# Optimization experiments

Measured on AMD Instinct MI355X. Metric: run time of the kernel, lower is better.

The kernel has to match this reference:

```python
import math
import jax, jax.numpy as jnp
import numpy as np

N = 2048          # batch size
D = 256           # embedding_dim
MEM = 16384       # memory_size
ANOMALY_WEIGHT = 1.0
TEMP = 0.1
MOMENTUM = 0.01
NCLS = 2          # binary phishing labels -> max(labels.max()+1, 2) == 2


def setup_inputs() -> dict:
    key = jax.random.key(0)
    ks = jax.random.split(key, 10)
    s = 1.0 / math.sqrt(D)  # nn.Linear default init range
    return {
        'z': jax.random.normal(ks[0], (N, D), jnp.float32),
        'labels': jax.random.randint(ks[1], (N,), 0, NCLS),
        'memory': jax.random.normal(ks[2], (MEM, D), jnp.float32),
        'memory_weights': jax.random.uniform(ks[3], (MEM,), jnp.float32),
        'running_mean': jnp.zeros((D,), jnp.float32),
        'running_cov': jnp.eye(D, dtype=jnp.float32),
        'Wq': jax.random.uniform(ks[4], (D, D), jnp.float32, -s, s),
        'bq': jax.random.uniform(ks[5], (D,), jnp.float32, -s, s),
        'Wk': jax.random.uniform(ks[6], (D, D), jnp.float32, -s, s),
        'bk': jax.random.uniform(ks[7], (D,), jnp.float32, -s, s),
        'Wv': jax.random.uniform(ks[8], (D, D), jnp.float32, -s, s),
        'bv': jax.random.uniform(ks[9], (D,), jnp.float32, -s, s),
    }


def reference(z, labels, memory, memory_weights, running_mean, running_cov,
              Wq, bq, Wk, bk, Wv, bv):
    # ---- update(z.detach(), labels): entire update path is detached in torch ----
    z_sg = jax.lax.stop_gradient(z)

    # _update_stats: EMA of batch mean / covariance (done before importance)
    mu = z_sg.mean(axis=0)                                  # [D]
    zc = z_sg - mu
    cov = zc.T @ zc / max(N - 1, 1)                         # [D, D]
    rm = (1.0 - MOMENTUM) * running_mean + MOMENTUM * mu
    rc = (1.0 - MOMENTUM) * running_cov + MOMENTUM * cov

    # _mahalanobis with updated running stats
    c = z_sg - rm
    cov_inv = jnp.linalg.inv(rc + 1e-6 * jnp.eye(D, dtype=rc.dtype))
    dist = jnp.sqrt(jnp.clip(jnp.einsum('nd,de,ne->n', c, cov_inv, c), 1e-8))
    a_norm = (dist - dist.min()) / (dist.max() - dist.min() + 1e-8)

    # _mi_proxy: KL(batch label dist || uniform), broadcast to all items
    counts = jnp.zeros((NCLS,), z.dtype).at[labels].add(1.0)
    p = counts / jnp.clip(counts.sum(), 1.0)
    # p / uniform == p * NCLS; clip inside log for safety (both classes present)
    kl = jnp.clip((p * jnp.log(jnp.clip(p * NCLS, 1e-8))).sum(), 0.0)
    importance = (1.0 + ANOMALY_WEIGHT * a_norm) * kl       # [N]

    # serial top-1 priority-queue eviction, in descending-importance order
    order = jnp.argsort(-importance)
    z_ord = z_sg[order]
    imp_ord = importance[order]

    def evict_step(state, inp):
        mem, w = state
        zi, imp = inp
        j = jnp.argmin(w)                   # weakest memory slot
        rep = imp > w[j]
        mem = mem.at[j].set(jnp.where(rep, zi, mem[j]))
        w = w.at[j].set(jnp.where(rep, imp, w[j]))
        return (mem, w), None

    (mem, _), _ = jax.lax.scan(evict_step, (memory, memory_weights), (z_ord, imp_ord))

    # ---- query(z): cross-attention over the (full) updated memory ----
    Q = z @ Wq.T + bq                       # [N, D]
    K = mem @ Wk.T + bk                     # [MEM, D]
    V = mem @ Wv.T + bv                     # [MEM, D]
    sc = (Q @ K.T) / math.sqrt(D)           # [N, MEM]
    attn = jax.nn.softmax(sc / TEMP, axis=-1)
    return z + 0.5 * (attn @ V)
```

## Files before the change

kernel.cpp:

```cpp
#include <hip/hip_runtime.h>
#include <math.h>

#define NB   2048
#define DE   256
#define MEMN 16384
#define CAND_CAP 256
#define FSPL 32
#define FKPS 512
#define FIT  16

typedef __attribute__((ext_vector_type(8)))  short  short8;
typedef __attribute__((ext_vector_type(16))) float  float16;
typedef __attribute__((ext_vector_type(4)))  unsigned uint4v;
typedef __attribute__((ext_vector_type(2)))  unsigned uint2v;

static const size_t OFF_QB   = 0;
static const size_t OFF_KB   = 262144;
static const size_t OFF_VTB  = 2359296;
static const size_t OFF_LP   = 4456448;
static const size_t OFF_OPB  = 4521984;
static const size_t SO_A    = 0;
static const size_t SO_X    = 65536;
static const size_t SO_MUP  = 131072;
static const size_t SO_DIST = 147456;

__device__ inline unsigned short f2bf(float f) {
  unsigned u = __float_as_uint(f);
  unsigned r = (u + 0x7fffu + ((u >> 16) & 1u)) >> 16;
  return (unsigned short)r;
}
__device__ inline float bf2f(unsigned short s) {
  return __uint_as_float((unsigned)s << 16);
}

__device__ inline unsigned cvtpk_bf16(float lo, float hi) {
  unsigned r;
  asm("v_cvt_pk_bf16_f32 %0, %1, %2" : "=v"(r) : "v"(lo), "v"(hi));
  return r;
}

__device__ inline void halfswap(unsigned& lo, unsigned& hi, int h) {
#if __has_builtin(__builtin_amdgcn_permlane32_swap)
  (void)h;
  uint2v r = __builtin_amdgcn_permlane32_swap(lo, hi, false, false);
  lo = r.x; hi = r.y;
#else
  unsigned a = (unsigned)__shfl_xor((int)lo, 32, 64);
  unsigned b = (unsigned)__shfl_xor((int)hi, 32, 64);
  unsigned nlo = (h == 0) ? lo : b;
  unsigned nhi = (h == 0) ? a  : hi;
  lo = nlo; hi = nhi;
#endif
}

__device__ inline void bitonic_sort_u64(unsigned long long* key, int n, int tid, int nth) {
  for (int k = 2; k <= n; k <<= 1) {
    for (int j = k >> 1; j > 0; j >>= 1) {
      __syncthreads();
      for (int i = tid; i < n; i += nth) {
        int ixj = i ^ j;
        if (ixj > i) {
          unsigned long long a = key[i], b = key[ixj];
          bool up = ((i & k) == 0);
          if ((a > b) == up) { key[i] = b; key[ixj] = a; }
        }
      }
    }
  }
  __syncthreads();
}

__global__ __launch_bounds__(256) void mupart_kernel(const float* __restrict__ z,
                                                     float* __restrict__ mup,
                                                     float* __restrict__ Az) {
  int d = threadIdx.x;
  int r0 = blockIdx.x * 32;
  float4 zero4 = {0.f, 0.f, 0.f, 0.f};
  *(float4*)&Az[(size_t)blockIdx.x * 1024 + threadIdx.x * 4] = zero4;
  float s = 0.f;
  for (int r = 0; r < 32; ++r) s += z[(size_t)(r0 + r) * DE + d];
  mup[blockIdx.x * DE + d] = s;
}

__global__ __launch_bounds__(256) void covpart_kernel(const float* __restrict__ z,
                                                      float* __restrict__ A) {
  __shared__ float As[16][68];
  __shared__ float Bs[16][68];
  int tid = threadIdx.x, tx = tid & 15, ty = tid >> 4;
  int i0 = blockIdx.x * 64, j0 = blockIdx.y * 64;
  int nbase = blockIdx.z * 128;
  float acc[4][4] = {};
  for (int nt = 0; nt < 8; ++nt) {
    int n0 = nbase + nt * 16;
    for (int e = tid; e < 1024; e += 256) {
      int c = e & 63, nn = e >> 6;
      As[nn][c] = z[(size_t)(n0 + nn) * DE + i0 + c];
      Bs[nn][c] = z[(size_t)(n0 + nn) * DE + j0 + c];
    }
    __syncthreads();
#pragma unroll
    for (int nn = 0; nn < 16; ++nn) {
      float4 a4 = *(const float4*)&As[nn][ty * 4];
      float4 b4 = *(const float4*)&Bs[nn][tx * 4];
      acc[0][0] += a4.x*b4.x; acc[0][1] += a4.x*b4.y; acc[0][2] += a4.x*b4.z; acc[0][3] += a4.x*b4.w;
      acc[1][0] += a4.y*b4.x; acc[1][1] += a4.y*b4.y; acc[1][2] += a4.y*b4.z; acc[1][3] += a4.y*b4.w;
      acc[2][0] += a4.z*b4.x; acc[2][1] += a4.z*b4.y; acc[2][2] += a4.z*b4.z; acc[2][3] += a4.z*b4.w;
      acc[3][0] += a4.w*b4.x; acc[3][1] += a4.w*b4.y; acc[3][2] += a4.w*b4.z; acc[3][3] += a4.w*b4.w;
    }
    __syncthreads();
  }
  for (int r = 0; r < 4; ++r) {
    int i = i0 + ty * 4 + r;
    for (int c = 0; c < 4; ++c) {
      int j = j0 + tx * 4 + c;
      atomicAdd(&A[(size_t)i * DE + j], acc[r][c]);
    }
  }
}

__global__ __launch_bounds__(256) void gemmx_kernel(const float* __restrict__ ZtZ,
                                                    const float* __restrict__ rcov,
                                                    const float* __restrict__ mup,
                                                    float* __restrict__ X) {
  __shared__ float Ea[16][17];
  __shared__ float Eb[16][17];
  __shared__ float mus[256];
  int t = threadIdx.x, tx = t & 15, ty = t >> 4;
  int i0 = blockIdx.x * 16, j0 = blockIdx.y * 16;
  {
    float s = 0.f;
    for (int b = 0; b < 64; ++b) s += mup[b * DE + t];
    mus[t] = s;
  }
  __syncthreads();
  const float c1 = 0.01f / (float)(NB - 1);
  const float invN = 1.0f / (float)NB;
  float acc = 0.f;
  for (int k0 = 0; k0 < 256; k0 += 16) {
    int c = k0 + tx;
    {
      int r = i0 + ty;
      float base = 0.99f * rcov[(size_t)r * DE + c] +
                   c1 * (ZtZ[(size_t)r * DE + c] - mus[r] * mus[c] * invN);
      float e = -base;
      if (r == c) e += 1.0f - 1e-6f;
      Ea[ty][tx] = e;
    }
    {
      int r = j0 + ty;
      float base = 0.99f * rcov[(size_t)r * DE + c] +
                   c1 * (ZtZ[(size_t)r * DE + c] - mus[r] * mus[c] * invN);
      float e = -base;
      if (r == c) e += 1.0f - 1e-6f;
      Eb[ty][tx] = e;
    }
    __syncthreads();
#pragma unroll
    for (int k = 0; k < 16; ++k) acc += Ea[ty][k] * Eb[tx][k];
    __syncthreads();
  }
  int r = i0 + ty, c = j0 + tx;
  float base = 0.99f * rcov[(size_t)r * DE + c] +
               c1 * (ZtZ[(size_t)r * DE + c] - mus[r] * mus[c] * invN);
  float e = -base;
  if (r == c) e += 1.0f - 1e-6f;
  X[(size_t)r * DE + c] = acc + e + ((r == c) ? 1.0f : 0.0f);
}

__global__ __launch_bounds__(256) void dist_kernel(const float* __restrict__ z,
                                                   const float* __restrict__ rmean,
                                                   const float* __restrict__ mup,
                                                   const float* __restrict__ X,
                                                   float* __restrict__ dist) {
  __shared__ float cc[4][256];
  __shared__ float4 red[256];
  int n0 = blockIdx.x * 4, i = threadIdx.x;
  float s = 0.f;
  for (int b = 0; b < 64; ++b) s += mup[b * DE + i];
  float rmi = 0.99f * rmean[i] + 0.01f * s * (1.0f / (float)NB);
#pragma unroll
  for (int r = 0; r < 4; ++r) cc[r][i] = z[(size_t)(n0 + r) * DE + i] - rmi;
  __syncthreads();
  float y0 = 0.f, y1 = 0.f, y2 = 0.f, y3 = 0.f;
#pragma unroll 8
  for (int j = 0; j < DE; ++j) {
    float x = X[(size_t)j * DE + i];
    y0 += x * cc[0][j]; y1 += x * cc[1][j]; y2 += x * cc[2][j]; y3 += x * cc[3][j];
  }
  float4 v;
  v.x = y0 * cc[0][i]; v.y = y1 * cc[1][i]; v.z = y2 * cc[2][i]; v.w = y3 * cc[3][i];
  red[i] = v;
  __syncthreads();
  for (int sH = 128; sH > 0; sH >>= 1) {
    if (i < sH) {
      float4 a = red[i], b = red[i + sH];
      a.x += b.x; a.y += b.y; a.z += b.z; a.w += b.w;
      red[i] = a;
    }
    __syncthreads();
  }
  if (i < 4) {
    float4 tt = red[0];
    float d = (i == 0) ? tt.x : (i == 1) ? tt.y : (i == 2) ? tt.z : tt.w;
    dist[n0 + i] = sqrtf(fmaxf(d, 1e-8f));
  }
}

__global__ __launch_bounds__(1024) void update_kernel(const float* __restrict__ dist,
                                                      const int* __restrict__ labels,
                                                      const float* __restrict__ weights,
                                                      const float* __restrict__ z,
                                                      float* __restrict__ memory) {
  __shared__ unsigned long long ikeys[NB];
  __shared__ unsigned long long ck[CAND_CAP];
  __shared__ unsigned long long gmin[16];
  __shared__ int slots[CAND_CAP], srcs[CAND_CAP];
  __shared__ float smin[16], smax[16];
  __shared__ int scnt[16];
  __shared__ float s_kl, s_dmin, s_inv;
  __shared__ int s_ccnt, s_m, s_stop, s_bg;
  int t = threadIdx.x;
  int wid = t >> 6, lane = t & 63;

  float mn = 1e30f, mx = -1e30f; int c1 = 0;
  for (int n = t; n < NB; n += 1024) {
    float d = dist[n];
    mn = fminf(mn, d); mx = fmaxf(mx, d);
    c1 += labels[n];
  }
#pragma unroll
  for (int o = 32; o > 0; o >>= 1) {
    mn = fminf(mn, __shfl_xor(mn, o, 64));
    mx = fmaxf(mx, __shfl_xor(mx, o, 64));
    c1 += __shfl_xor(c1, o, 64);
  }
  if (lane == 0) { smin[wid] = mn; smax[wid] = mx; scnt[wid] = c1; }
  if (t == 0) { s_ccnt = 0; s_m = 0; s_stop = 0; }
  __syncthreads();
  if (t == 0) {
    float a = 1e30f, b = -1e30f; int cc = 0;
    for (int i = 0; i < 16; ++i) { a = fminf(a, smin[i]); b = fmaxf(b, smax[i]); cc += scnt[i]; }
    float p1 = (float)cc / (float)NB;
    float p0 = (float)(NB - cc) / (float)NB;
    float kl = p0 * logf(fmaxf(2.f * p0, 1e-8f)) + p1 * logf(fmaxf(2.f * p1, 1e-8f));
    s_kl = fmaxf(kl, 0.f);
    s_dmin = a;
    s_inv = 1.0f / (b - a + 1e-8f);
  }
  __syncthreads();
  float kl = s_kl;

  for (int n = t; n < NB; n += 1024) {
    float imp = (1.0f + (dist[n] - s_dmin) * s_inv) * kl;
    ikeys[n] = ((unsigned long long)(unsigned)(~__float_as_uint(imp)) << 32) | (unsigned)n;
  }
  float thresh = 2.f * kl;
  for (int j = t; j < MEMN; j += 1024) {
    float wv = weights[j];
    if (wv < thresh) {
      int p = atomicAdd(&s_ccnt, 1);
      if (p < CAND_CAP) ck[p] = ((unsigned long long)__float_as_uint(wv) << 32) | (unsigned)j;
    }
  }
  __syncthreads();
  int C = s_ccnt; if (C > CAND_CAP) C = CAND_CAP;
  for (int i = t; i < CAND_CAP; i += 1024)
    if (i >= C) ck[i] = 0xFFFFFFFFFFFFFFFFULL;
  bitonic_sort_u64(ck, CAND_CAP, t, 1024);

  {
    unsigned long long a = ikeys[wid * 128 + lane];
    unsigned long long b = ikeys[wid * 128 + 64 + lane];
    unsigned long long mm = a < b ? a : b;
#pragma unroll
    for (int o = 32; o > 0; o >>= 1) {
      unsigned long long ot = (unsigned long long)__shfl_xor((long long)mm, o, 64);
      if (ot < mm) mm = ot;
    }
    if (lane == 0) gmin[wid] = mm;
  }
  __syncthreads();

  float prevv = 0.f;
  for (int i = 0; i < C; ++i) {
    if (t == 0) {
      unsigned long long best = 0xFFFFFFFFFFFFFFFFULL;
      for (int g = 0; g < 16; ++g) if (gmin[g] < best) best = gmin[g];
      float im = __uint_as_float(~(unsigned)(best >> 32));
      float wv = __uint_as_float((unsigned)(ck[i] >> 32));
      bool ok = (im > wv) && (i == 0 || prevv >= wv);
      if (ok) {
        int idx = (int)(best & 0xffffffffULL);
        slots[s_m] = (int)(ck[i] & 0xffffffffULL);
        srcs[s_m]  = idx;
        s_m++;
        prevv = im;
        ikeys[idx] = 0xFFFFFFFFFFFFFFFFULL;
        s_bg = idx >> 7;
      } else {
        s_stop = 1; s_bg = -1;
      }
    }
    __syncthreads();
    if (s_stop) break;
    if (wid == s_bg) {
      unsigned long long a = ikeys[wid * 128 + lane];
      unsigned long long b = ikeys[wid * 128 + 64 + lane];
      unsigned long long mm = a < b ? a : b;
#pragma unroll
      for (int o = 32; o > 0; o >>= 1) {
        unsigned long long ot = (unsigned long long)__shfl_xor((long long)mm, o, 64);
        if (ot < mm) mm = ot;
      }
      if (lane == 0) gmin[wid] = mm;
    }
    __syncthreads();
  }
  int m = s_m;
  for (int e = t; e < m * DE; e += 1024) {
    int i = e >> 8, d = e & 255;
    memory[(size_t)slots[i] * DE + d] = z[(size_t)srcs[i] * DE + d];
  }
}

__global__ __launch_bounds__(256, 1) void qkv_kernel(
    const float* __restrict__ z, const float* __restrict__ memory,
    const float* __restrict__ Wq, const float* __restrict__ bq,
    const float* __restrict__ Wk, const float* __restrict__ bk,
    const float* __restrict__ Wv, const float* __restrict__ bv,
    unsigned short* __restrict__ Qbf, unsigned short* __restrict__ Kbf,
    unsigned short* __restrict__ Vtb) {
  __shared__ unsigned short Bsh[64 * 264];
  int flat = blockIdx.x;
  const float *Af, *Bf, *bias;
  unsigned short* C;
  int bias_row, vtile, gx, gy, ldC;
  if (flat < 64) {
    gx = flat & 15; gy = flat >> 4;
    Af = z; Bf = Wq; bias = bq; bias_row = 0; vtile = 0; C = Qbf; ldC = DE;
  } else if (flat < 576) {
    int f = flat - 64; gx = f & 127; gy = f >> 7;
    Af = memory; Bf = Wk; bias = bk; bias_row = 0; vtile = 0; C = Kbf; ldC = DE;
  } else {
    int f = flat - 576; gx = f & 1; gy = f >> 1;
    Af = Wv; Bf = memory; bias = bv; bias_row = 1; vtile = 1; C = Vtb; ldC = 0;
  }

  int tid = threadIdx.x;
  int w = tid >> 6, lane = tid & 63;
  int m = lane & 31, h = lane >> 5;
  int arow = gx * 128 + w * 32 + m;
  int n0 = gy * 64;

  short8 af[16];
#pragma unroll
  for (int kc = 0; kc < 16; ++kc) {
    const float* src = &Af[(size_t)arow * DE + kc * 16 + h * 8];
    float4 f0 = *(const float4*)&src[0];
    float4 f1 = *(const float4*)&src[4];
    short8 v;
    v[0] = (short)f2bf(f0.x); v[1] = (short)f2bf(f0.y);
    v[2] = (short)f2bf(f0.z); v[3] = (short)f2bf(f0.w);
    v[4] = (short)f2bf(f1.x); v[5] = (short)f2bf(f1.y);
    v[6] = (short)f2bf(f1.z); v[7] = (short)f2bf(f1.w);
    af[kc] = v;
  }
  {
    int r = tid >> 2, q = tid & 3;
    const float* src = &Bf[(size_t)(n0 + r) * DE + q * 64];
    unsigned short* dst = &Bsh[r * 264 + q * 64];
#pragma unroll
    for (int j = 0; j < 8; ++j) {
      float4 f0 = *(const float4*)&src[j * 8];
      float4 f1 = *(const float4*)&src[j * 8 + 4];
      short8 v;
      v[0] = (short)f2bf(f0.x); v[1] = (short)f2bf(f0.y);
      v[2] = (short)f2bf(f0.z); v[3] = (short)f2bf(f0.w);
      v[4] = (short)f2bf(f1.x); v[5] = (short)f2bf(f1.y);
      v[6] = (short)f2bf(f1.z); v[7] = (short)f2bf(f1.w);
      *(short8*)&dst[j * 8] = v;
    }
  }
  __syncthreads();

  float16 a0 = {}, a1 = {};
#pragma unroll
  for (int kc = 0; kc < 16; ++kc) {
    short8 b0 = *(const short8*)&Bsh[(0 * 32 + m) * 264 + kc * 16 + h * 8];
    short8 b1 = *(const short8*)&Bsh[(1 * 32 + m) * 264 + kc * 16 + h * 8];
    a0 = __builtin_amdgcn_mfma_f32_32x32x16_bf16(af[kc], b0, a0, 0, 0, 0);
    a1 = __builtin_amdgcn_mfma_f32_32x32x16_bf16(af[kc], b1, a1, 0, 0, 0);
  }
#pragma unroll
  for (int r = 0; r < 16; ++r) {
    int rr = (r & 3) + 8 * (r >> 2) + 4 * h;
    int orow = gx * 128 + w * 32 + rr;
    int oc0 = n0 + m, oc1 = n0 + 32 + m;
    float bb0 = bias_row ? bias[orow] : bias[oc0];
    float bb1 = bias_row ? bias[orow] : bias[oc1];
    if (!vtile) {
      C[(size_t)orow * ldC + oc0] = f2bf(a0[r] + bb0);
      C[(size_t)orow * ldC + oc1] = f2bf(a1[r] + bb1);
    } else {
      C[(size_t)(oc0 >> 5) * 8192 + (size_t)orow * 32 + (oc0 & 31)] = f2bf(a0[r] + bb0);
      C[(size_t)(oc1 >> 5) * 8192 + (size_t)orow * 32 + (oc1 & 31)] = f2bf(a1[r] + bb1);
    }
  }
}

__global__ __launch_bounds__(512, 2) void flash_kernel(
    const unsigned short* __restrict__ Qb, const unsigned short* __restrict__ Kb,
    const unsigned short* __restrict__ Vtb, unsigned short* __restrict__ Opb,
    float* __restrict__ Lp) {
  __shared__ unsigned short Ks[32 * 264];
  __shared__ unsigned short Vs[256 * 40];

  int tid = threadIdx.x;
  int w = tid >> 6, lane = tid & 63;
  int m = lane & 31, h = lane >> 5;
  int sp = blockIdx.x, qg = blockIdx.y;
  int myrow = qg * 256 + w * 32 + m;

  short8 qf[16];
#pragma unroll
  for (int kc = 0; kc < 16; ++kc)
    qf[kc] = *(const short8*)&Qb[(size_t)myrow * DE + kc * 16 + h * 8];

  float16 O[8] = {};
  float lacc = 0.f;

  short8 kreg[2], vreg[2];
#define LOAD_TILES(kb_)                                                              \
  {                                                                                  \
    int kb = (kb_);                                                                  \
    _Pragma("unroll")                                                                \
    for (int i = 0; i < 2; ++i) {                                                    \
      int c = i * 512 + tid, kr = c >> 5, kcol = c & 31;                             \
      kreg[i] = *(const short8*)&Kb[(size_t)(kb + kr) * DE + kcol * 8];              \
    }                                                                                \
    const unsigned short* vg = &Vtb[(size_t)((kb) >> 5) * 8192];                     \
    _Pragma("unroll")                                                                \
    for (int i = 0; i < 2; ++i) {                                                    \
      int c = i * 512 + tid;                                                         \
      vreg[i] = *(const short8*)&vg[c * 8];                                          \
    }                                                                                \
  }
#define STORE_TILES()                                                                \
  {                                                                                  \
    _Pragma("unroll")                                                                \
    for (int i = 0; i < 2; ++i) {                                                    \
      int c = i * 512 + tid, kr = c >> 5, kcol = c & 31;                             \
      *(short8*)&Ks[kr * 264 + kcol * 8] = kreg[i];                                  \
    }                                                                                \
    _Pragma("unroll")                                                                \
    for (int i = 0; i < 2; ++i) {                                                    \
      int c = i * 512 + tid, dr = c >> 2, dc = c & 3;                                \
      *(short8*)&Vs[dr * 40 + dc * 8] = vreg[i];                                     \
    }                                                                                \
  }

  LOAD_TILES(sp * FKPS);

  for (int it = 0; it < FIT; ++it) {
    __syncthreads();
    STORE_TILES();
    if (it + 1 < FIT) LOAD_TILES(sp * FKPS + (it + 1) * 32);
    __syncthreads();

    float16 s = {};
    __builtin_amdgcn_s_setprio(1);
#pragma unroll
    for (int kc = 0; kc < 16; ++kc) {
      short8 b0 = *(const short8*)&Ks[m * 264 + kc * 16 + h * 8];
      s = __builtin_amdgcn_mfma_f32_32x32x16_bf16(b0, qf[kc], s, 0, 0, 0);
    }
    __builtin_amdgcn_s_setprio(0);

    float p[16];
#pragma unroll
    for (int r = 0; r < 16; ++r)
      p[r] = exp2f(fmaf(s[r], 0.90168440f, -16.0f));

    lacc += ((p[0] + p[1]) + (p[2] + p[3])) + ((p[4] + p[5]) + (p[6] + p[7])) +
            ((p[8] + p[9]) + (p[10] + p[11])) + ((p[12] + p[13]) + (p[14] + p[15]));

    unsigned c0 = cvtpk_bf16(p[0],  p[1]);
    unsigned c1 = cvtpk_bf16(p[2],  p[3]);
    unsigned c2 = cvtpk_bf16(p[4],  p[5]);
    unsigned c3 = cvtpk_bf16(p[6],  p[7]);
    unsigned c4 = cvtpk_bf16(p[8],  p[9]);
    unsigned c5 = cvtpk_bf16(p[10], p[11]);
    unsigned c6 = cvtpk_bf16(p[12], p[13]);
    unsigned c7 = cvtpk_bf16(p[14], p[15]);
    halfswap(c0, c2, h);
    halfswap(c1, c3, h);
    halfswap(c4, c6, h);
    halfswap(c5, c7, h);
    uint4v w0v = {c0, c1, c2, c3};
    uint4v w1v = {c4, c5, c6, c7};
    short8 pa0 = __builtin_bit_cast(short8, w0v);
    short8 pa1 = __builtin_bit_cast(short8, w1v);

    __builtin_amdgcn_s_setprio(1);
#pragma unroll
    for (int ct = 0; ct < 8; ++ct) {
      short8 vb0 = *(const short8*)&Vs[(ct * 32 + m) * 40 + h * 8];
      short8 vb1 = *(const short8*)&Vs[(ct * 32 + m) * 40 + 16 + h * 8];
      O[ct] = __builtin_amdgcn_mfma_f32_32x32x16_bf16(pa0, vb0, O[ct], 0, 0, 0);
      O[ct] = __builtin_amdgcn_mfma_f32_32x32x16_bf16(pa1, vb1, O[ct], 0, 0, 0);
    }
    __builtin_amdgcn_s_setprio(0);
  }
#undef LOAD_TILES
#undef STORE_TILES

  size_t ob = ((size_t)sp * NB + qg * 256 + w * 32) * DE;
#pragma unroll
  for (int ct = 0; ct < 8; ++ct)
#pragma unroll
    for (int r = 0; r < 16; ++r) {
      int rr = (r & 3) + 8 * (r >> 2) + 4 * h;
      Opb[ob + (size_t)rr * DE + ct * 32 + m] = f2bf(O[ct][r]);
    }
  float ltot = lacc + __shfl_xor(lacc, 32, 64);
  if (h == 0)
    Lp[sp * NB + qg * 256 + w * 32 + m] = ltot;
}

__global__ __launch_bounds__(256) void combine_kernel(const float* __restrict__ z,
                                                      const unsigned short* __restrict__ Opb,
                                                      const float* __restrict__ Lp,
                                                      float* __restrict__ out) {
  int n = blockIdx.x, c = threadIdx.x;
  float num = 0.f, den = 0.f;
#pragma unroll
  for (int s = 0; s < FSPL; ++s) {
    den += Lp[s * NB + n];
    num += bf2f(Opb[((size_t)s * NB + n) * DE + c]);
  }
  size_t base = (size_t)n * DE + c;
  out[base] = z[base] + 0.5f * num / den;
}

extern "C" void kernel_launch(void* const* d_in, const int* in_sizes, int n_in,
                              void* d_out, int out_size, void* d_ws, size_t ws_size,
                              hipStream_t stream) {
  (void)in_sizes; (void)n_in; (void)out_size; (void)ws_size;
  const float* z       = (const float*)d_in[0];
  const int*   labels  = (const int*)d_in[1];
  float*       memory  = (float*)d_in[2];
  const float* weights = (const float*)d_in[3];
  const float* rmean   = (const float*)d_in[4];
  const float* rcov    = (const float*)d_in[5];
  const float* Wq      = (const float*)d_in[6];
  const float* bq      = (const float*)d_in[7];
  const float* Wk      = (const float*)d_in[8];
  const float* bk      = (const float*)d_in[9];
  const float* Wv      = (const float*)d_in[10];
  const float* bv      = (const float*)d_in[11];
  float* out = (float*)d_out;
  float* ws  = (float*)d_ws;

  unsigned short* Qbf = (unsigned short*)(ws + OFF_QB);
  unsigned short* Kbf = (unsigned short*)(ws + OFF_KB);
  unsigned short* Vtb = (unsigned short*)(ws + OFF_VTB);
  float* Lp           = ws + OFF_LP;
  unsigned short* Opb = (unsigned short*)(ws + OFF_OPB);
  float* SB    = ws + OFF_OPB;
  float* A     = SB + SO_A;
  float* X     = SB + SO_X;
  float* mup   = SB + SO_MUP;
  float* dist  = SB + SO_DIST;

  mupart_kernel<<<64, 256, 0, stream>>>(z, mup, A);
  covpart_kernel<<<dim3(4, 4, 16), 256, 0, stream>>>(z, A);
  gemmx_kernel<<<dim3(16, 16), 256, 0, stream>>>(A, rcov, mup, X);
  dist_kernel<<<NB / 4, 256, 0, stream>>>(z, rmean, mup, X, dist);
  update_kernel<<<1, 1024, 0, stream>>>(dist, labels, weights, z, memory);
  qkv_kernel<<<1088, 256, 0, stream>>>(z, memory, Wq, bq, Wk, bk, Wv, bv, Qbf, Kbf, Vtb);
  flash_kernel<<<dim3(FSPL, NB / 256), 512, 0, stream>>>(Qbf, Kbf, Vtb, Opb, Lp);
  combine_kernel<<<NB, 256, 0, stream>>>(z, Opb, Lp, out);
}
```

Measured before the change: 241.4 us.

## Swizzle K tile in LDS, rank-sort small candidate sets, pack bf16 conversions

Three separate changes. The flash kernel's K tile in shared memory drops its row padding in favour of an XOR swizzle on column offsets, which avoids bank conflicts and saves LDS. The eviction kernel replaces the 256-element bitonic sort with a single-wavefront rank sort when there are at most 64 candidates. The projection kernel converts fp32 to bf16 with packed hardware convert instructions instead of per-element software rounding. The small-candidate path adds an extra barrier and only runs when the candidate count is small.

```diff
diff --git a/kernel.cpp b/kernel.cpp
--- a/kernel.cpp
+++ b/kernel.cpp
@@ -37,6 +37,11 @@
   unsigned r;
   asm("v_cvt_pk_bf16_f32 %0, %1, %2" : "=v"(r) : "v"(lo), "v"(hi));
   return r;
+}
+__device__ inline short8 pack8_bf16(float4 f0, float4 f1) {
+  uint4v u = {cvtpk_bf16(f0.x, f0.y), cvtpk_bf16(f0.z, f0.w),
+              cvtpk_bf16(f1.x, f1.y), cvtpk_bf16(f1.z, f1.w)};
+  return __builtin_bit_cast(short8, u);
 }
 
 __device__ inline void halfswap(unsigned& lo, unsigned& hi, int h) {
@@ -266,7 +271,21 @@
   int C = s_ccnt; if (C > CAND_CAP) C = CAND_CAP;
   for (int i = t; i < CAND_CAP; i += 1024)
     if (i >= C) ck[i] = 0xFFFFFFFFFFFFFFFFULL;
-  bitonic_sort_u64(ck, CAND_CAP, t, 1024);
+  __syncthreads();
+  if (C <= 64) {
+    if (wid == 0) {
+      unsigned long long key = (lane < C) ? ck[lane] : 0xFFFFFFFFFFFFFFFFULL;
+      int rank = 0;
+      for (int j = 0; j < 64; ++j) {
+        unsigned long long o = (unsigned long long)__shfl((long long)key, j, 64);
+        rank += (o < key) || (o == key && j < lane);
+      }
+      if (lane < C) ck[rank] = key;
+    }
+    __syncthreads();
+  } else {
+    bitonic_sort_u64(ck, CAND_CAP, t, 1024);
+  }
 
   {
     unsigned long long a = ikeys[wid * 128 + lane];
@@ -358,12 +377,7 @@
     const float* src = &Af[(size_t)arow * DE + kc * 16 + h * 8];
     float4 f0 = *(const float4*)&src[0];
     float4 f1 = *(const float4*)&src[4];
-    short8 v;
-    v[0] = (short)f2bf(f0.x); v[1] = (short)f2bf(f0.y);
-    v[2] = (short)f2bf(f0.z); v[3] = (short)f2bf(f0.w);
-    v[4] = (short)f2bf(f1.x); v[5] = (short)f2bf(f1.y);
-    v[6] = (short)f2bf(f1.z); v[7] = (short)f2bf(f1.w);
-    af[kc] = v;
+    af[kc] = pack8_bf16(f0, f1);
   }
   {
     int r = tid >> 2, q = tid & 3;
@@ -373,12 +387,7 @@
     for (int j = 0; j < 8; ++j) {
       float4 f0 = *(const float4*)&src[j * 8];
       float4 f1 = *(const float4*)&src[j * 8 + 4];
-      short8 v;
-      v[0] = (short)f2bf(f0.x); v[1] = (short)f2bf(f0.y);
-      v[2] = (short)f2bf(f0.z); v[3] = (short)f2bf(f0.w);
-      v[4] = (short)f2bf(f1.x); v[5] = (short)f2bf(f1.y);
-      v[6] = (short)f2bf(f1.z); v[7] = (short)f2bf(f1.w);
-      *(short8*)&dst[j * 8] = v;
+      *(short8*)&dst[j * 8] = pack8_bf16(f0, f1);
     }
   }
   __syncthreads();
@@ -412,7 +421,7 @@
     const unsigned short* __restrict__ Qb, const unsigned short* __restrict__ Kb,
     const unsigned short* __restrict__ Vtb, unsigned short* __restrict__ Opb,
     float* __restrict__ Lp) {
-  __shared__ unsigned short Ks[32 * 264];
+  __shared__ unsigned short Ks[32 * 256];
   __shared__ unsigned short Vs[256 * 40];
 
   int tid = threadIdx.x;
@@ -450,7 +459,7 @@
     _Pragma("unroll")                                                                \
     for (int i = 0; i < 2; ++i) {                                                    \
       int c = i * 512 + tid, kr = c >> 5, kcol = c & 31;                             \
-      *(short8*)&Ks[kr * 264 + kcol * 8] = kreg[i];                                  \
+      *(short8*)&Ks[kr * 256 + ((kcol * 8) ^ ((kr & 7) << 3))] = kreg[i];            \
     }                                                                                \
     _Pragma("unroll")                                                                \
     for (int i = 0; i < 2; ++i) {                                                    \
@@ -471,7 +480,7 @@
     __builtin_amdgcn_s_setprio(1);
 #pragma unroll
     for (int kc = 0; kc < 16; ++kc) {
-      short8 b0 = *(const short8*)&Ks[m * 264 + kc * 16 + h * 8];
+      short8 b0 = *(const short8*)&Ks[m * 256 + ((kc * 16 + h * 8) ^ ((m & 7) << 3))];
       s = __builtin_amdgcn_mfma_f32_32x32x16_bf16(b0, qf[kc], s, 0, 0, 0);
     }
     __builtin_amdgcn_s_setprio(0);
```

Result: slower. 256.6 us (+6.3%).
